# Optimization experiments

Hardware: AMD Instinct MI355X
Metric: run time of the kernel (lower is better)

## Reference

```python
import jax, jax.numpy as jnp
import numpy as np

N_NODES = 100000
N_EDGES = 3200000
_EPS = 1e-6

# SE3 layout: [tx, ty, tz, qx, qy, qz, qw] (pypose convention)

def _normalize_se3(T):
    t, q = T[..., :3], T[..., 3:7]
    q = q / jnp.linalg.norm(q, axis=-1, keepdims=True)
    return jnp.concatenate([t, q], axis=-1)

def _qmul(q, r):
    qx, qy, qz, qw = q[..., 0], q[..., 1], q[..., 2], q[..., 3]
    rx, ry, rz, rw = r[..., 0], r[..., 1], r[..., 2], r[..., 3]
    x = qw * rx + qx * rw + qy * rz - qz * ry
    y = qw * ry - qx * rz + qy * rw + qz * rx
    z = qw * rz + qx * ry - qy * rx + qz * rw
    w = qw * rw - qx * rx - qy * ry - qz * rz
    return jnp.stack([x, y, z, w], axis=-1)

def _qrot(q, v):
    # rotate vector v by unit quaternion q: v + 2 w (u x v) + 2 u x (u x v)
    u, w = q[..., :3], q[..., 3:4]
    t = 2.0 * jnp.cross(u, v)
    return v + w * t + jnp.cross(u, t)

def _se3_inv(T):
    t, q = T[..., :3], T[..., 3:7]
    qc = q * jnp.asarray([-1.0, -1.0, -1.0, 1.0], dtype=T.dtype)
    ti = -_qrot(qc, t)
    return jnp.concatenate([ti, qc], axis=-1)

def _se3_mul(A, B):
    ta, qa = A[..., :3], A[..., 3:7]
    tb, qb = B[..., :3], B[..., 3:7]
    return jnp.concatenate([ta + _qrot(qa, tb), _qmul(qa, qb)], axis=-1)

def _so3_log(q):
    # quaternion (xyzw) -> axis-angle 3-vector
    v, w = q[..., :3], q[..., 3]
    n = jnp.linalg.norm(v, axis=-1)
    n_safe = jnp.where(n > _EPS, n, 1.0)
    scale = jnp.where(n > _EPS, 2.0 * jnp.arctan2(n, w) / n_safe, 2.0 / jnp.where(jnp.abs(w) > _EPS, w, 1.0))
    return v * scale[..., None]

def _se3_log(T):
    # SE3 -> se3 = [tau(3), phi(3)], tau = Jl(phi)^{-1} t
    t, q = T[..., :3], T[..., 3:7]
    phi = _so3_log(q)
    theta = jnp.linalg.norm(phi, axis=-1)
    small = theta < _EPS
    th = jnp.where(small, 1.0, theta)
    c = jnp.where(small, 1.0 / 12.0, 1.0 / th**2 - (1.0 + jnp.cos(th)) / (2.0 * th * jnp.sin(th)))
    pxt = jnp.cross(phi, t)
    tau = t - 0.5 * pxt + c[..., None] * jnp.cross(phi, pxt)
    return jnp.concatenate([tau, phi], axis=-1)

def setup_inputs() -> dict:
    key = jax.random.key(0)
    k1, k2, k3 = jax.random.split(key, 3)
    nodes = _normalize_se3(jax.random.normal(k1, (N_NODES, 7), dtype=jnp.float32))
    poses = _normalize_se3(jax.random.normal(k2, (N_EDGES, 7), dtype=jnp.float32))
    edges = jax.random.randint(k3, (N_EDGES, 2), 0, N_NODES, dtype=jnp.int64)
    return {"edges": edges, "poses": poses, "nodes": nodes}

def reference(edges, poses, nodes):
    node1 = nodes[edges[..., 0]]  # [E, 7]
    node2 = nodes[edges[..., 1]]  # [E, 7]
    error = _se3_mul(_se3_mul(_se3_inv(poses), node2), _se3_inv(node1))
    return _se3_log(error)  # [E, 6]
```

## Files before the change

kernel.cpp:

```cpp
#include <hip/hip_runtime.h>
#include <math.h>

#define BLOCK 256
#define EPS 1e-6f

struct F3 { float x, y, z; };
struct F4 { float x, y, z, w; };

__device__ __forceinline__ F3 cross3(F3 a, F3 b) {
    return F3{a.y * b.z - a.z * b.y,
              a.z * b.x - a.x * b.z,
              a.x * b.y - a.y * b.x};
}

__device__ __forceinline__ F3 add3(F3 a, F3 b) { return F3{a.x + b.x, a.y + b.y, a.z + b.z}; }
__device__ __forceinline__ F3 neg3(F3 a) { return F3{-a.x, -a.y, -a.z}; }

__device__ __forceinline__ F3 qrot(F4 q, F3 v) {
    F3 u{q.x, q.y, q.z};
    F3 t = cross3(u, v);
    t.x *= 2.0f; t.y *= 2.0f; t.z *= 2.0f;
    F3 c = cross3(u, t);
    return F3{v.x + q.w * t.x + c.x,
              v.y + q.w * t.y + c.y,
              v.z + q.w * t.z + c.z};
}

__device__ __forceinline__ F4 qmul(F4 q, F4 r) {
    return F4{
        q.w * r.x + q.x * r.w + q.y * r.z - q.z * r.y,
        q.w * r.y - q.x * r.z + q.y * r.w + q.z * r.x,
        q.w * r.z + q.x * r.y - q.y * r.x + q.z * r.w,
        q.w * r.w - q.x * r.x - q.y * r.y - q.z * r.z};
}

__global__ void __launch_bounds__(BLOCK) pose_graph_kernel(
    const int* __restrict__ edges,
    const float* __restrict__ poses,
    const float* __restrict__ nodes,
    float* __restrict__ out,
    int n)
{
    __shared__ float sp[BLOCK * 7];
    __shared__ float so[BLOCK * 6];

    const int tid = threadIdx.x;
    const long long base = (long long)blockIdx.x * BLOCK;
    const int limit = (int)min((long long)BLOCK, (long long)n - base);

    {
        const float* psrc = poses + base * 7;
        const int tot = limit * 7;
        #pragma unroll
        for (int k = 0; k < 7; ++k) {
            int idx = tid + k * BLOCK;
            if (idx < tot) sp[idx] = psrc[idx];
        }
    }
    __syncthreads();

    if (tid < limit) {
        const long long e = base + tid;

        const int2 ed = ((const int2*)edges)[e];

        const float* p = &sp[tid * 7];
        F3 tp{p[0], p[1], p[2]};
        F4 qp{p[3], p[4], p[5], p[6]};

        const float* n1p = nodes + (size_t)ed.x * 7;
        const float* n2p = nodes + (size_t)ed.y * 7;
        F3 t1{n1p[0], n1p[1], n1p[2]};
        F4 q1{n1p[3], n1p[4], n1p[5], n1p[6]};
        F3 t2{n2p[0], n2p[1], n2p[2]};
        F4 q2{n2p[3], n2p[4], n2p[5], n2p[6]};

        F4 qpc{-qp.x, -qp.y, -qp.z, qp.w};
        F3 tpi = neg3(qrot(qpc, tp));

        F3 tA = add3(tpi, qrot(qpc, t2));
        F4 qA = qmul(qpc, q2);

        F4 q1c{-q1.x, -q1.y, -q1.z, q1.w};
        F3 t1i = neg3(qrot(q1c, t1));

        F3 tE = add3(tA, qrot(qA, t1i));
        F4 qE = qmul(qA, q1c);

        F3 v{qE.x, qE.y, qE.z};
        float w = qE.w;
        float nn = sqrtf(v.x * v.x + v.y * v.y + v.z * v.z);
        float n_safe = (nn > EPS) ? nn : 1.0f;
        float w_safe = (fabsf(w) > EPS) ? w : 1.0f;
        float scale = (nn > EPS) ? (2.0f * atan2f(nn, w) / n_safe)
                                 : (2.0f / w_safe);
        F3 phi{v.x * scale, v.y * scale, v.z * scale};

        float theta2 = phi.x * phi.x + phi.y * phi.y + phi.z * phi.z;
        float theta = sqrtf(theta2);
        bool small = theta < EPS;
        float th = small ? 1.0f : theta;
        float s, cth;
        sincosf(th, &s, &cth);
        float c = small ? (1.0f / 12.0f)
                        : (1.0f / (th * th) - (1.0f + cth) / (2.0f * th * s));
        F3 pxt = cross3(phi, tE);
        F3 ppxt = cross3(phi, pxt);
        F3 tau{tE.x - 0.5f * pxt.x + c * ppxt.x,
               tE.y - 0.5f * pxt.y + c * ppxt.y,
               tE.z - 0.5f * pxt.z + c * ppxt.z};

        float* o = &so[tid * 6];
        o[0] = tau.x; o[1] = tau.y; o[2] = tau.z;
        o[3] = phi.x; o[4] = phi.y; o[5] = phi.z;
    }
    __syncthreads();

    {
        float* odst = out + base * 6;
        const int tot = limit * 6;
        #pragma unroll
        for (int k = 0; k < 6; ++k) {
            int idx = tid + k * BLOCK;
            if (idx < tot) odst[idx] = so[idx];
        }
    }
}

extern "C" void kernel_launch(void* const* d_in, const int* in_sizes, int n_in,
                              void* d_out, int out_size, void* d_ws, size_t ws_size,
                              hipStream_t stream) {
    const int* edges = (const int*)d_in[0];
    const float* poses = (const float*)d_in[1];
    const float* nodes = (const float*)d_in[2];
    float* out = (float*)d_out;

    const int n_edges = in_sizes[0] / 2;
    const int grid = (n_edges + BLOCK - 1) / BLOCK;

    pose_graph_kernel<<<grid, BLOCK, 0, stream>>>(edges, poses, nodes, out, n_edges);
}
```

Baseline: 229.4 us.

## Repack nodes to 8-float stride for vectorized gathers and vectorize pose/output copies

Adds a pre-pass kernel that copies the node table into a 32-byte-aligned 8-float layout in workspace, so each node gather becomes two float4 loads instead of seven scalar loads. Full blocks also stage poses into shared memory and write outputs with float4 accesses instead of scalar ones. The aim is to cut the number of memory transactions for the random node gathers and the streaming traffic. In exchange it adds an extra kernel launch and writes the repacked table on every call, and keeps a scalar fallback kernel for when the workspace is too small.

Result: faster. 220.9 us (-3.7%).

```diff
diff --git a/kernel.cpp b/kernel.cpp
--- a/kernel.cpp
+++ b/kernel.cpp
@@ -12,7 +12,6 @@
               a.z * b.x - a.x * b.z,
               a.x * b.y - a.y * b.x};
 }
-
 __device__ __forceinline__ F3 add3(F3 a, F3 b) { return F3{a.x + b.x, a.y + b.y, a.z + b.z}; }
 __device__ __forceinline__ F3 neg3(F3 a) { return F3{-a.x, -a.y, -a.z}; }
 
@@ -25,7 +24,6 @@
               v.y + q.w * t.y + c.y,
               v.z + q.w * t.z + c.z};
 }
-
 __device__ __forceinline__ F4 qmul(F4 q, F4 r) {
     return F4{
         q.w * r.x + q.x * r.w + q.y * r.z - q.z * r.y,
@@ -34,96 +32,152 @@
         q.w * r.w - q.x * r.x - q.y * r.y - q.z * r.z};
 }
 
+__global__ void __launch_bounds__(BLOCK) repack_nodes_kernel(
+    const float* __restrict__ nodes, float* __restrict__ nodes8, int total7)
+{
+    int idx = blockIdx.x * BLOCK + threadIdx.x;
+    int stride = gridDim.x * BLOCK;
+    for (; idx < total7; idx += stride) {
+        int node = idx / 7;
+        int comp = idx - node * 7;
+        nodes8[node * 8 + comp] = nodes[idx];
+    }
+}
+
+__device__ __forceinline__ void compute_edge(
+    const float* __restrict__ p,
+    F3 t1, F4 q1, F3 t2, F4 q2,
+    float* __restrict__ o)
+{
+    F3 tp{p[0], p[1], p[2]};
+    F4 qp{p[3], p[4], p[5], p[6]};
+
+    F4 qpc{-qp.x, -qp.y, -qp.z, qp.w};
+    F3 tpi = neg3(qrot(qpc, tp));
+
+    F3 tA = add3(tpi, qrot(qpc, t2));
+    F4 qA = qmul(qpc, q2);
+
+    F4 q1c{-q1.x, -q1.y, -q1.z, q1.w};
+    F3 t1i = neg3(qrot(q1c, t1));
+
+    F3 tE = add3(tA, qrot(qA, t1i));
+    F4 qE = qmul(qA, q1c);
+
+    F3 v{qE.x, qE.y, qE.z};
+    float w = qE.w;
+    float nn = sqrtf(v.x * v.x + v.y * v.y + v.z * v.z);
+    float n_safe = (nn > EPS) ? nn : 1.0f;
+    float w_safe = (fabsf(w) > EPS) ? w : 1.0f;
+    float scale = (nn > EPS) ? (2.0f * atan2f(nn, w) / n_safe)
+                             : (2.0f / w_safe);
+    F3 phi{v.x * scale, v.y * scale, v.z * scale};
+
+    float theta2 = phi.x * phi.x + phi.y * phi.y + phi.z * phi.z;
+    float theta = sqrtf(theta2);
+    bool small = theta < EPS;
+    float th = small ? 1.0f : theta;
+    float s, cth;
+    sincosf(th, &s, &cth);
+    float c = small ? (1.0f / 12.0f)
+                    : (1.0f / (th * th) - (1.0f + cth) / (2.0f * th * s));
+    F3 pxt = cross3(phi, tE);
+    F3 ppxt = cross3(phi, pxt);
+    o[0] = tE.x - 0.5f * pxt.x + c * ppxt.x;
+    o[1] = tE.y - 0.5f * pxt.y + c * ppxt.y;
+    o[2] = tE.z - 0.5f * pxt.z + c * ppxt.z;
+    o[3] = phi.x; o[4] = phi.y; o[5] = phi.z;
+}
+
 __global__ void __launch_bounds__(BLOCK) pose_graph_kernel(
     const int* __restrict__ edges,
     const float* __restrict__ poses,
-    const float* __restrict__ nodes,
+    const float* __restrict__ nodes8,
     float* __restrict__ out,
     int n)
 {
-    __shared__ float sp[BLOCK * 7];
-    __shared__ float so[BLOCK * 6];
+    __shared__ float4 sp4[(BLOCK * 7 + 3) / 4];
+    __shared__ float  so[BLOCK * 6];
 
     const int tid = threadIdx.x;
     const long long base = (long long)blockIdx.x * BLOCK;
     const int limit = (int)min((long long)BLOCK, (long long)n - base);
-
+    float* sp = (float*)sp4;
+
+    if (limit == BLOCK) {
+        const float4* psrc = (const float4*)(poses + base * 7);
+        sp4[tid] = psrc[tid];
+        if (tid < (BLOCK * 7 / 4) - BLOCK)
+            sp4[tid + BLOCK] = psrc[tid + BLOCK];
+    } else {
+        const float* psrc = poses + base * 7;
+        const int tot = limit * 7;
+        for (int idx = tid; idx < tot; idx += BLOCK) sp[idx] = psrc[idx];
+    }
+    __syncthreads();
+
+    if (tid < limit) {
+        const long long e = base + tid;
+        const int2 ed = ((const int2*)edges)[e];
+
+        const float4* n1p = (const float4*)(nodes8 + (size_t)ed.x * 8);
+        const float4* n2p = (const float4*)(nodes8 + (size_t)ed.y * 8);
+        float4 a1 = n1p[0], b1 = n1p[1];
+        float4 a2 = n2p[0], b2 = n2p[1];
+
+        F3 t1{a1.x, a1.y, a1.z};
+        F4 q1{a1.w, b1.x, b1.y, b1.z};
+        F3 t2{a2.x, a2.y, a2.z};
+        F4 q2{a2.w, b2.x, b2.y, b2.z};
+
+        compute_edge(&sp[tid * 7], t1, q1, t2, q2, &so[tid * 6]);
+    }
+    __syncthreads();
+
+    if (limit == BLOCK) {
+        float4* odst = (float4*)(out + base * 6);
+        float4* sov = (float4*)so;
+        odst[tid] = sov[tid];
+        if (tid < (BLOCK * 6 / 4) - BLOCK)
+            odst[tid + BLOCK] = sov[tid + BLOCK];
+    } else {
+        float* odst = out + base * 6;
+        const int tot = limit * 6;
+        for (int idx = tid; idx < tot; idx += BLOCK) odst[idx] = so[idx];
+    }
+}
+
+__global__ void __launch_bounds__(BLOCK) pose_graph_kernel_fallback(
+    const int* __restrict__ edges, const float* __restrict__ poses,
+    const float* __restrict__ nodes, float* __restrict__ out, int n)
+{
+    __shared__ float sp[BLOCK * 7];
+    __shared__ float so[BLOCK * 6];
+    const int tid = threadIdx.x;
+    const long long base = (long long)blockIdx.x * BLOCK;
+    const int limit = (int)min((long long)BLOCK, (long long)n - base);
     {
         const float* psrc = poses + base * 7;
         const int tot = limit * 7;
-        #pragma unroll
-        for (int k = 0; k < 7; ++k) {
-            int idx = tid + k * BLOCK;
-            if (idx < tot) sp[idx] = psrc[idx];
-        }
-    }
-    __syncthreads();
-
+        for (int idx = tid; idx < tot; idx += BLOCK) sp[idx] = psrc[idx];
+    }
+    __syncthreads();
     if (tid < limit) {
         const long long e = base + tid;
-
         const int2 ed = ((const int2*)edges)[e];
-
-        const float* p = &sp[tid * 7];
-        F3 tp{p[0], p[1], p[2]};
-        F4 qp{p[3], p[4], p[5], p[6]};
-
         const float* n1p = nodes + (size_t)ed.x * 7;
         const float* n2p = nodes + (size_t)ed.y * 7;
         F3 t1{n1p[0], n1p[1], n1p[2]};
         F4 q1{n1p[3], n1p[4], n1p[5], n1p[6]};
         F3 t2{n2p[0], n2p[1], n2p[2]};
         F4 q2{n2p[3], n2p[4], n2p[5], n2p[6]};
-
-        F4 qpc{-qp.x, -qp.y, -qp.z, qp.w};
-        F3 tpi = neg3(qrot(qpc, tp));
-
-        F3 tA = add3(tpi, qrot(qpc, t2));
-        F4 qA = qmul(qpc, q2);
-
-        F4 q1c{-q1.x, -q1.y, -q1.z, q1.w};
-        F3 t1i = neg3(qrot(q1c, t1));
-
-        F3 tE = add3(tA, qrot(qA, t1i));
-        F4 qE = qmul(qA, q1c);
-
-        F3 v{qE.x, qE.y, qE.z};
-        float w = qE.w;
-        float nn = sqrtf(v.x * v.x + v.y * v.y + v.z * v.z);
-        float n_safe = (nn > EPS) ? nn : 1.0f;
-        float w_safe = (fabsf(w) > EPS) ? w : 1.0f;
-        float scale = (nn > EPS) ? (2.0f * atan2f(nn, w) / n_safe)
-                                 : (2.0f / w_safe);
-        F3 phi{v.x * scale, v.y * scale, v.z * scale};
-
-        float theta2 = phi.x * phi.x + phi.y * phi.y + phi.z * phi.z;
-        float theta = sqrtf(theta2);
-        bool small = theta < EPS;
-        float th = small ? 1.0f : theta;
-        float s, cth;
-        sincosf(th, &s, &cth);
-        float c = small ? (1.0f / 12.0f)
-                        : (1.0f / (th * th) - (1.0f + cth) / (2.0f * th * s));
-        F3 pxt = cross3(phi, tE);
-        F3 ppxt = cross3(phi, pxt);
-        F3 tau{tE.x - 0.5f * pxt.x + c * ppxt.x,
-               tE.y - 0.5f * pxt.y + c * ppxt.y,
-               tE.z - 0.5f * pxt.z + c * ppxt.z};
-
-        float* o = &so[tid * 6];
-        o[0] = tau.x; o[1] = tau.y; o[2] = tau.z;
-        o[3] = phi.x; o[4] = phi.y; o[5] = phi.z;
-    }
-    __syncthreads();
-
+        compute_edge(&sp[tid * 7], t1, q1, t2, q2, &so[tid * 6]);
+    }
+    __syncthreads();
     {
         float* odst = out + base * 6;
         const int tot = limit * 6;
-        #pragma unroll
-        for (int k = 0; k < 6; ++k) {
-            int idx = tid + k * BLOCK;
-            if (idx < tot) odst[idx] = so[idx];
-        }
+        for (int idx = tid; idx < tot; idx += BLOCK) odst[idx] = so[idx];
     }
 }
 
@@ -136,7 +190,17 @@
     float* out = (float*)d_out;
 
     const int n_edges = in_sizes[0] / 2;
+    const int n_nodes = in_sizes[2] / 7;
     const int grid = (n_edges + BLOCK - 1) / BLOCK;
 
-    pose_graph_kernel<<<grid, BLOCK, 0, stream>>>(edges, poses, nodes, out, n_edges);
-}
+    const size_t ws_needed = (size_t)n_nodes * 8 * sizeof(float);
+    if (ws_size >= ws_needed) {
+        float* nodes8 = (float*)d_ws;
+        const int total7 = n_nodes * 7;
+        const int rgrid = (total7 + BLOCK - 1) / BLOCK;
+        repack_nodes_kernel<<<rgrid, BLOCK, 0, stream>>>(nodes, nodes8, total7);
+        pose_graph_kernel<<<grid, BLOCK, 0, stream>>>(edges, poses, nodes8, out, n_edges);
+    } else {
+        pose_graph_kernel_fallback<<<grid, BLOCK, 0, stream>>>(edges, poses, nodes, out, n_edges);
+    }
+}
```
